# Optimization experiments

Hardware: AMD Instinct MI355X
Metric: run time of the kernel (lower is better)

The kernel has to match this reference:

```python
import jax, jax.numpy as jnp
import numpy as np

EPS = 1e-6

def setup_inputs() -> dict:
    key = jax.random.key(0)
    k1, k2 = jax.random.split(key)
    shape = (20, 1, 128, 128, 128)
    # BCE requires x strictly in (0,1); keep away from endpoints like a sigmoid output.
    x = jax.random.uniform(k1, shape, dtype=jnp.float32, minval=EPS, maxval=1.0 - EPS)
    y = jax.random.uniform(k2, shape, dtype=jnp.float32, minval=0.0, maxval=1.0)
    return {"x": x, "y": y}

def reference(x, y):
    # binary_cross_entropy (mean reduction); torch clamps log terms at -100
    log_x = jnp.clip(jnp.log(x), -100.0)
    log_1mx = jnp.clip(jnp.log1p(-x), -100.0)
    mseloss = -jnp.mean(y * log_x + (1.0 - y) * log_1mx)

    # threshold prediction at 0.5 -> {0,1}; truncate target to int (floor toward 0)
    xb = jnp.where(x > 0.5, 1, 0)              # int
    yb = y.astype(jnp.int32)                   # astype(int) truncation

    B = x.shape[0]  # loop is over range(20); batch == 20
    por_pred = jnp.mean((xb == 0).astype(jnp.float32).reshape(B, -1), axis=1)
    por_true = jnp.mean((yb == 0).astype(jnp.float32).reshape(B, -1), axis=1)
    PORE = jnp.mean((por_pred - por_true) ** 2)  # sum over 20 samples / 20

    return (PORE + mseloss, PORE)
```

## Files before the change

kernel.cpp:

```cpp
#include <hip/hip_runtime.h>

#define NBATCH 20
#define ELEMS_PER_BATCH (128 * 128 * 128)
#define BLOCKS_PER_BATCH 128
#define THREADS 256
#define V4_PER_THREAD 16
#define NPART (NBATCH * BLOCKS_PER_BATCH)

#define LN2 0.69314718055994530942
#define LOG2_CLAMP (-144.26950408889634f)

__global__ __launch_bounds__(THREADS) void partial_kernel(
    const float* __restrict__ x, const float* __restrict__ y,
    float* __restrict__ bce_part, int* __restrict__ pred_part,
    int* __restrict__ true_part) {
  const int b   = blockIdx.y;
  const int seg = blockIdx.x;
  const int tid = threadIdx.x;

  const long base4 = (long)b * (ELEMS_PER_BATCH / 4) +
                     (long)seg * (THREADS * V4_PER_THREAD);
  const float4* __restrict__ x4 = (const float4*)x;
  const float4* __restrict__ y4 = (const float4*)y;

  float bce2 = 0.0f;
  int pc = 0, tc = 0;

#pragma unroll
  for (int k = 0; k < V4_PER_THREAD; ++k) {
    const long idx = base4 + (long)k * THREADS + tid;
    const float4 xv = x4[idx];
    const float4 yv = y4[idx];

#pragma unroll
    for (int c = 0; c < 4; ++c) {
      const float xx = (c == 0) ? xv.x : (c == 1) ? xv.y : (c == 2) ? xv.z : xv.w;
      const float yy = (c == 0) ? yv.x : (c == 1) ? yv.y : (c == 2) ? yv.z : yv.w;
      const float lx = fmaxf(__builtin_amdgcn_logf(xx),        LOG2_CLAMP);
      const float l1 = fmaxf(__builtin_amdgcn_logf(1.0f - xx), LOG2_CLAMP);
      bce2 += l1 + yy * (lx - l1);
      pc += (xx <= 0.5f);
      tc += (yy < 1.0f);
    }
  }

  __shared__ float sb[THREADS];
  __shared__ int   sp[THREADS];
  __shared__ int   st[THREADS];
  sb[tid] = bce2; sp[tid] = pc; st[tid] = tc;
  __syncthreads();
#pragma unroll
  for (int s = THREADS / 2; s > 0; s >>= 1) {
    if (tid < s) {
      sb[tid] += sb[tid + s];
      sp[tid] += sp[tid + s];
      st[tid] += st[tid + s];
    }
    __syncthreads();
  }
  if (tid == 0) {
    const int o = b * BLOCKS_PER_BATCH + seg;
    bce_part[o]  = (float)(sb[0] * LN2);
    pred_part[o] = sp[0];
    true_part[o] = st[0];
  }
}

__global__ __launch_bounds__(THREADS) void final_kernel(
    const float* __restrict__ bce_part, const int* __restrict__ pred_part,
    const int* __restrict__ true_part, float* __restrict__ out) {
  const int tid = threadIdx.x;
  __shared__ double sred[THREADS];
  __shared__ float  spor[NBATCH];

  double local = 0.0;
  for (int i = tid; i < NPART; i += THREADS) local += (double)bce_part[i];
  sred[tid] = local;
  __syncthreads();
#pragma unroll
  for (int s = THREADS / 2; s > 0; s >>= 1) {
    if (tid < s) sred[tid] += sred[tid + s];
    __syncthreads();
  }

  if (tid < NBATCH) {
    int pc = 0, tc = 0;
    for (int k = 0; k < BLOCKS_PER_BATCH; ++k) {
      pc += pred_part[tid * BLOCKS_PER_BATCH + k];
      tc += true_part[tid * BLOCKS_PER_BATCH + k];
    }
    const float pp = (float)pc / (float)ELEMS_PER_BATCH;
    const float pt = (float)tc / (float)ELEMS_PER_BATCH;
    const float d = pp - pt;
    spor[tid] = d * d;
  }
  __syncthreads();

  if (tid == 0) {
    float pore_sum = 0.0f;
#pragma unroll
    for (int b = 0; b < NBATCH; ++b) pore_sum += spor[b];
    const float pore = pore_sum / (float)NBATCH;
    const double total = (double)NBATCH * (double)ELEMS_PER_BATCH;
    const float mse = (float)(-(sred[0] / total));
    out[0] = pore + mse;
    out[1] = pore;
  }
}

extern "C" void kernel_launch(void* const* d_in, const int* in_sizes, int n_in,
                              void* d_out, int out_size, void* d_ws, size_t ws_size,
                              hipStream_t stream) {
  const float* x = (const float*)d_in[0];
  const float* y = (const float*)d_in[1];
  float* out = (float*)d_out;

  float* bce_part  = (float*)d_ws;
  int*   pred_part = (int*)(bce_part + NPART);
  int*   true_part = pred_part + NPART;

  dim3 grid(BLOCKS_PER_BATCH, NBATCH);
  partial_kernel<<<grid, THREADS, 0, stream>>>(x, y, bce_part, pred_part, true_part);
  final_kernel<<<1, THREADS, 0, stream>>>(bce_part, pred_part, true_part, out);
}
```

Before: 338.4 us.

## Double-buffer register loads and halve blocks per batch

Each block now processes twice as much data (64 blocks per batch, 32 float4 per thread). The loads go through an explicit two-buffer register pipeline: the next batch of four float4 pairs is issued before the current batch is computed. The intent is to overlap memory latency with the log computation and to cut per-block reduction overhead. In exchange there are fewer blocks in flight and register pressure rises, which may reduce occupancy.

```diff
diff --git a/kernel.cpp b/kernel.cpp
--- a/kernel.cpp
+++ b/kernel.cpp
@@ -2,13 +2,44 @@
 
 #define NBATCH 20
 #define ELEMS_PER_BATCH (128 * 128 * 128)
-#define BLOCKS_PER_BATCH 128
+#define BLOCKS_PER_BATCH 64
 #define THREADS 256
-#define V4_PER_THREAD 16
+#define BAT 4
+#define NSTEP 8
 #define NPART (NBATCH * BLOCKS_PER_BATCH)
 
 #define LN2 0.69314718055994530942
 #define LOG2_CLAMP (-144.26950408889634f)
+
+__device__ __forceinline__ void load_batch(const float4* __restrict__ x4,
+                                           const float4* __restrict__ y4,
+                                           long base, int tid,
+                                           float4 (&bx)[BAT], float4 (&by)[BAT]) {
+#pragma unroll
+  for (int j = 0; j < BAT; ++j) {
+    const long idx = base + (long)j * THREADS + tid;
+    bx[j] = x4[idx];
+    by[j] = y4[idx];
+  }
+}
+
+__device__ __forceinline__ void compute_batch(const float4 (&bx)[BAT],
+                                              const float4 (&by)[BAT],
+                                              float& bce2, int& pc, int& tc) {
+#pragma unroll
+  for (int j = 0; j < BAT; ++j) {
+#pragma unroll
+    for (int c = 0; c < 4; ++c) {
+      const float xx = (c == 0) ? bx[j].x : (c == 1) ? bx[j].y : (c == 2) ? bx[j].z : bx[j].w;
+      const float yy = (c == 0) ? by[j].x : (c == 1) ? by[j].y : (c == 2) ? by[j].z : by[j].w;
+      const float lx = fmaxf(__builtin_amdgcn_logf(xx),        LOG2_CLAMP);
+      const float l1 = fmaxf(__builtin_amdgcn_logf(1.0f - xx), LOG2_CLAMP);
+      bce2 += l1 + yy * (lx - l1);
+      pc += (xx <= 0.5f);
+      tc += (yy < 1.0f);
+    }
+  }
+}
 
 __global__ __launch_bounds__(THREADS) void partial_kernel(
     const float* __restrict__ x, const float* __restrict__ y,
@@ -19,30 +50,30 @@
   const int tid = threadIdx.x;
 
   const long base4 = (long)b * (ELEMS_PER_BATCH / 4) +
-                     (long)seg * (THREADS * V4_PER_THREAD);
+                     (long)seg * (BAT * NSTEP * THREADS);
   const float4* __restrict__ x4 = (const float4*)x;
   const float4* __restrict__ y4 = (const float4*)y;
 
   float bce2 = 0.0f;
   int pc = 0, tc = 0;
 
-#pragma unroll
-  for (int k = 0; k < V4_PER_THREAD; ++k) {
-    const long idx = base4 + (long)k * THREADS + tid;
-    const float4 xv = x4[idx];
-    const float4 yv = y4[idx];
+  float4 ax[BAT], ay[BAT], bx[BAT], by[BAT];
+  load_batch(x4, y4, base4, tid, ax, ay);
 
-#pragma unroll
-    for (int c = 0; c < 4; ++c) {
-      const float xx = (c == 0) ? xv.x : (c == 1) ? xv.y : (c == 2) ? xv.z : xv.w;
-      const float yy = (c == 0) ? yv.x : (c == 1) ? yv.y : (c == 2) ? yv.z : yv.w;
-      const float lx = fmaxf(__builtin_amdgcn_logf(xx),        LOG2_CLAMP);
-      const float l1 = fmaxf(__builtin_amdgcn_logf(1.0f - xx), LOG2_CLAMP);
-      bce2 += l1 + yy * (lx - l1);
-      pc += (xx <= 0.5f);
-      tc += (yy < 1.0f);
-    }
-  }
+#define PIPE_STEP(CX, CY, NX, NY, S)                                           \
+  if ((S) + 1 < NSTEP)                                                         \
+    load_batch(x4, y4, base4 + (long)((S) + 1) * (BAT * THREADS), tid, NX, NY);\
+  compute_batch(CX, CY, bce2, pc, tc);
+
+  PIPE_STEP(ax, ay, bx, by, 0)
+  PIPE_STEP(bx, by, ax, ay, 1)
+  PIPE_STEP(ax, ay, bx, by, 2)
+  PIPE_STEP(bx, by, ax, ay, 3)
+  PIPE_STEP(ax, ay, bx, by, 4)
+  PIPE_STEP(bx, by, ax, ay, 5)
+  PIPE_STEP(ax, ay, bx, by, 6)
+  PIPE_STEP(bx, by, ax, ay, 7)
+#undef PIPE_STEP
 
   __shared__ float sb[THREADS];
   __shared__ int   sp[THREADS];
```

Result: no change. 337.4 us (-0.3%).

## Restructure partial reduction to stride across batches with software-pipelined nontemporal loads

Applied to the files above, without the earlier changes.

Each thread now handles one float4 position in every one of the 20 batches. It double-buffers the loads so the next batch's data is fetched while the current batch is computed, and the loads use nontemporal hints. Per-batch counts are packed into one int, reduced within each wavefront by shuffles, and summed through shared-memory atomics. The final kernel is reworked to sum the packed per-batch partials. This is meant to improve memory-level parallelism and cut shared-memory reduction work, at the cost of more partials and atomics and strided batch access.

```diff
diff --git a/kernel.cpp b/kernel.cpp
--- a/kernel.cpp
+++ b/kernel.cpp
@@ -2,79 +2,94 @@
 
 #define NBATCH 20
 #define ELEMS_PER_BATCH (128 * 128 * 128)
-#define BLOCKS_PER_BATCH 128
+#define BATCH_F4 (ELEMS_PER_BATCH / 4)
 #define THREADS 256
-#define V4_PER_THREAD 16
-#define NPART (NBATCH * BLOCKS_PER_BATCH)
+#define GRID_BLOCKS 2048
 
 #define LN2 0.69314718055994530942
 #define LOG2_CLAMP (-144.26950408889634f)
 
-__global__ __launch_bounds__(THREADS) void partial_kernel(
+typedef float f4 __attribute__((ext_vector_type(4)));
+
+
+__global__ __launch_bounds__(THREADS, 8) void partial_kernel(
     const float* __restrict__ x, const float* __restrict__ y,
-    float* __restrict__ bce_part, int* __restrict__ pred_part,
-    int* __restrict__ true_part) {
-  const int b   = blockIdx.y;
-  const int seg = blockIdx.x;
+    float* __restrict__ bce_part, int* __restrict__ comb_part) {
   const int tid = threadIdx.x;
+  const int gid = blockIdx.x * THREADS + tid;
 
-  const long base4 = (long)b * (ELEMS_PER_BATCH / 4) +
-                     (long)seg * (THREADS * V4_PER_THREAD);
-  const float4* __restrict__ x4 = (const float4*)x;
-  const float4* __restrict__ y4 = (const float4*)y;
+  const f4* __restrict__ x4 = (const f4*)x;
+  const f4* __restrict__ y4 = (const f4*)y;
+
+  __shared__ int sc[NBATCH];
+  if (tid < NBATCH) sc[tid] = 0;
+  __syncthreads();
 
   float bce2 = 0.0f;
-  int pc = 0, tc = 0;
 
-#pragma unroll
-  for (int k = 0; k < V4_PER_THREAD; ++k) {
-    const long idx = base4 + (long)k * THREADS + tid;
-    const float4 xv = x4[idx];
-    const float4 yv = y4[idx];
+  f4 xa, ya, xb, yb;
+  xa = __builtin_nontemporal_load(&x4[gid]);
+  ya = __builtin_nontemporal_load(&y4[gid]);
 
-#pragma unroll
-    for (int c = 0; c < 4; ++c) {
-      const float xx = (c == 0) ? xv.x : (c == 1) ? xv.y : (c == 2) ? xv.z : xv.w;
-      const float yy = (c == 0) ? yv.x : (c == 1) ? yv.y : (c == 2) ? yv.z : yv.w;
-      const float lx = fmaxf(__builtin_amdgcn_logf(xx),        LOG2_CLAMP);
-      const float l1 = fmaxf(__builtin_amdgcn_logf(1.0f - xx), LOG2_CLAMP);
-      bce2 += l1 + yy * (lx - l1);
-      pc += (xx <= 0.5f);
-      tc += (yy < 1.0f);
-    }
+#define PROCESS(XV, YV, S)                                                     \
+  {                                                                            \
+    int pc = 0, tc = 0;                                                        \
+    _Pragma("unroll")                                                          \
+    for (int c = 0; c < 4; ++c) {                                              \
+      const float xx = XV[c];                                                  \
+      const float yy = YV[c];                                                  \
+      const float lx = fmaxf(__builtin_amdgcn_logf(xx),        LOG2_CLAMP);    \
+      const float l1 = fmaxf(__builtin_amdgcn_logf(1.0f - xx), LOG2_CLAMP);    \
+      bce2 += l1 + yy * (lx - l1);                          \
+      pc += (xx <= 0.5f);                                                      \
+      tc += (yy < 1.0f);                                                       \
+    }                                                                          \
+    int packed = pc | (tc << 16); \
+    _Pragma("unroll")                                                          \
+    for (int o = 32; o > 0; o >>= 1) packed += __shfl_xor(packed, o);          \
+    if ((tid & 63) == 0) atomicAdd(&sc[S], packed);                            \
   }
 
+#define STEP(CX, CY, NX, NY, S)                                                \
+  if ((S) + 1 < NBATCH) {                                                      \
+    NX = __builtin_nontemporal_load(&x4[((S) + 1) * BATCH_F4 + gid]);          \
+    NY = __builtin_nontemporal_load(&y4[((S) + 1) * BATCH_F4 + gid]);          \
+  }                                                                            \
+  PROCESS(CX, CY, S)
+
+  STEP(xa, ya, xb, yb, 0)   STEP(xb, yb, xa, ya, 1)
+  STEP(xa, ya, xb, yb, 2)   STEP(xb, yb, xa, ya, 3)
+  STEP(xa, ya, xb, yb, 4)   STEP(xb, yb, xa, ya, 5)
+  STEP(xa, ya, xb, yb, 6)   STEP(xb, yb, xa, ya, 7)
+  STEP(xa, ya, xb, yb, 8)   STEP(xb, yb, xa, ya, 9)
+  STEP(xa, ya, xb, yb, 10)  STEP(xb, yb, xa, ya, 11)
+  STEP(xa, ya, xb, yb, 12)  STEP(xb, yb, xa, ya, 13)
+  STEP(xa, ya, xb, yb, 14)  STEP(xb, yb, xa, ya, 15)
+  STEP(xa, ya, xb, yb, 16)  STEP(xb, yb, xa, ya, 17)
+  STEP(xa, ya, xb, yb, 18)  STEP(xb, yb, xa, ya, 19)
+#undef STEP
+#undef PROCESS
+
   __shared__ float sb[THREADS];
-  __shared__ int   sp[THREADS];
-  __shared__ int   st[THREADS];
-  sb[tid] = bce2; sp[tid] = pc; st[tid] = tc;
+  sb[tid] = bce2;
   __syncthreads();
 #pragma unroll
   for (int s = THREADS / 2; s > 0; s >>= 1) {
-    if (tid < s) {
-      sb[tid] += sb[tid + s];
-      sp[tid] += sp[tid + s];
-      st[tid] += st[tid + s];
-    }
+    if (tid < s) sb[tid] += sb[tid + s];
     __syncthreads();
   }
-  if (tid == 0) {
-    const int o = b * BLOCKS_PER_BATCH + seg;
-    bce_part[o]  = (float)(sb[0] * LN2);
-    pred_part[o] = sp[0];
-    true_part[o] = st[0];
-  }
+  if (tid == 0) bce_part[blockIdx.x] = sb[0] * (float)LN2;
+  if (tid < NBATCH) comb_part[tid * GRID_BLOCKS + blockIdx.x] = sc[tid];
 }
 
 __global__ __launch_bounds__(THREADS) void final_kernel(
-    const float* __restrict__ bce_part, const int* __restrict__ pred_part,
-    const int* __restrict__ true_part, float* __restrict__ out) {
+    const float* __restrict__ bce_part, const int* __restrict__ comb_part,
+    float* __restrict__ out) {
   const int tid = threadIdx.x;
+
   __shared__ double sred[THREADS];
-  __shared__ float  spor[NBATCH];
-
   double local = 0.0;
-  for (int i = tid; i < NPART; i += THREADS) local += (double)bce_part[i];
+  for (int i = tid; i < GRID_BLOCKS; i += THREADS) local += (double)bce_part[i];
   sred[tid] = local;
   __syncthreads();
 #pragma unroll
@@ -83,14 +98,30 @@
     __syncthreads();
   }
 
+  __shared__ int pcb[NBATCH], tcb[NBATCH];
+  if (tid < NBATCH) { pcb[tid] = 0; tcb[tid] = 0; }
+  __syncthreads();
+  for (int s = 0; s < NBATCH; ++s) {
+    int pl = 0, tl = 0;
+    for (int i = tid; i < GRID_BLOCKS; i += THREADS) {
+      const int c = comb_part[s * GRID_BLOCKS + i];
+      pl += c & 0xFFFF;
+      tl += (c >> 16) & 0xFFFF;
+    }
+    long long packed = (long long)pl | ((long long)tl << 32);
+#pragma unroll
+    for (int o = 32; o > 0; o >>= 1) packed += __shfl_xor(packed, o);
+    if ((tid & 63) == 0) {
+      atomicAdd(&pcb[s], (int)(packed & 0xFFFFFFFFll));
+      atomicAdd(&tcb[s], (int)(packed >> 32));
+    }
+  }
+  __syncthreads();
+
+  __shared__ float spor[NBATCH];
   if (tid < NBATCH) {
-    int pc = 0, tc = 0;
-    for (int k = 0; k < BLOCKS_PER_BATCH; ++k) {
-      pc += pred_part[tid * BLOCKS_PER_BATCH + k];
-      tc += true_part[tid * BLOCKS_PER_BATCH + k];
-    }
-    const float pp = (float)pc / (float)ELEMS_PER_BATCH;
-    const float pt = (float)tc / (float)ELEMS_PER_BATCH;
+    const float pp = (float)pcb[tid] / (float)ELEMS_PER_BATCH;
+    const float pt = (float)tcb[tid] / (float)ELEMS_PER_BATCH;
     const float d = pp - pt;
     spor[tid] = d * d;
   }
@@ -116,10 +147,8 @@
   float* out = (float*)d_out;
 
   float* bce_part  = (float*)d_ws;
-  int*   pred_part = (int*)(bce_part + NPART);
-  int*   true_part = pred_part + NPART;
+  int*   comb_part = (int*)(bce_part + GRID_BLOCKS);
 
-  dim3 grid(BLOCKS_PER_BATCH, NBATCH);
-  partial_kernel<<<grid, THREADS, 0, stream>>>(x, y, bce_part, pred_part, true_part);
-  final_kernel<<<1, THREADS, 0, stream>>>(bce_part, pred_part, true_part, out);
+  partial_kernel<<<GRID_BLOCKS, THREADS, 0, stream>>>(x, y, bce_part, comb_part);
+  final_kernel<<<1, THREADS, 0, stream>>>(bce_part, comb_part, out);
 }
```

New measurement: 435.1 us. 28.6% more time.

## Double-buffer global-to-LDS async loads and use wave-shuffle block reduction

Applied to the files above, without the earlier changes.

Each block now covers twice the data (64 blocks per batch) and streams x and y through a double-buffered LDS tile using global_load_lds direct-to-LDS copies, with explicit vmcnt waits so the loads of tile t+2 overlap the compute on tile t. The shared-memory tree reduction is replaced by wave-level shuffles followed by a four-entry cross-wave combine that reuses the tile buffers. The aim is to keep more memory traffic in flight and cut the cost of the reduction. The risks are fewer blocks in the grid, more LDS per block lowering occupancy, and the extra LDS round-trip. Correctness also depends on the hand-written waitcnt counts being right.

```diff
diff --git a/kernel.cpp b/kernel.cpp
--- a/kernel.cpp
+++ b/kernel.cpp
@@ -2,13 +2,22 @@
 
 #define NBATCH 20
 #define ELEMS_PER_BATCH (128 * 128 * 128)
-#define BLOCKS_PER_BATCH 128
+#define BLOCKS_PER_BATCH 64
 #define THREADS 256
-#define V4_PER_THREAD 16
+#define TILE_F4 512
+#define NTILE 16
 #define NPART (NBATCH * BLOCKS_PER_BATCH)
 
 #define LN2 0.69314718055994530942
 #define LOG2_CLAMP (-144.26950408889634f)
+
+typedef float f4 __attribute__((ext_vector_type(4)));
+typedef const __attribute__((address_space(1))) unsigned int gu32;
+typedef __attribute__((address_space(3)))       unsigned int lu32;
+
+__device__ __forceinline__ void stage16(const f4* g, f4* l) {
+  __builtin_amdgcn_global_load_lds((gu32*)g, (lu32*)l, 16, 0, 2);
+}
 
 __global__ __launch_bounds__(THREADS) void partial_kernel(
     const float* __restrict__ x, const float* __restrict__ y,
@@ -19,50 +28,91 @@
   const int tid = threadIdx.x;
 
   const long base4 = (long)b * (ELEMS_PER_BATCH / 4) +
-                     (long)seg * (THREADS * V4_PER_THREAD);
-  const float4* __restrict__ x4 = (const float4*)x;
-  const float4* __restrict__ y4 = (const float4*)y;
+                     (long)seg * (NTILE * TILE_F4);
+  const f4* __restrict__ x4 = (const f4*)x;
+  const f4* __restrict__ y4 = (const f4*)y;
+
+  __shared__ f4 lx[2][TILE_F4];
+  __shared__ f4 ly[2][TILE_F4];
 
   float bce2 = 0.0f;
   int pc = 0, tc = 0;
 
-#pragma unroll
-  for (int k = 0; k < V4_PER_THREAD; ++k) {
-    const long idx = base4 + (long)k * THREADS + tid;
-    const float4 xv = x4[idx];
-    const float4 yv = y4[idx];
-
-#pragma unroll
-    for (int c = 0; c < 4; ++c) {
-      const float xx = (c == 0) ? xv.x : (c == 1) ? xv.y : (c == 2) ? xv.z : xv.w;
-      const float yy = (c == 0) ? yv.x : (c == 1) ? yv.y : (c == 2) ? yv.z : yv.w;
-      const float lx = fmaxf(__builtin_amdgcn_logf(xx),        LOG2_CLAMP);
-      const float l1 = fmaxf(__builtin_amdgcn_logf(1.0f - xx), LOG2_CLAMP);
-      bce2 += l1 + yy * (lx - l1);
-      pc += (xx <= 0.5f);
-      tc += (yy < 1.0f);
-    }
+#define STAGE(T, B)                                                            \
+  {                                                                            \
+    const long tb = base4 + (long)(T) * TILE_F4;                               \
+    stage16(&x4[tb + tid],       &lx[B][tid]);                                 \
+    stage16(&x4[tb + 256 + tid], &lx[B][256 + tid]);                           \
+    stage16(&y4[tb + tid],       &ly[B][tid]);                                 \
+    stage16(&y4[tb + 256 + tid], &ly[B][256 + tid]);                           \
   }
 
-  __shared__ float sb[THREADS];
-  __shared__ int   sp[THREADS];
-  __shared__ int   st[THREADS];
-  sb[tid] = bce2; sp[tid] = pc; st[tid] = tc;
+#define PH(T, B, VM)                                                           \
+  asm volatile("s_waitcnt vmcnt(" #VM ")" ::: "memory");                       \
+  __builtin_amdgcn_sched_barrier(0);                                           \
+  {                                                                            \
+    _Pragma("unroll")                                                          \
+    for (int j = 0; j < 2; ++j) {                                              \
+      const f4 xv = lx[B][j * 256 + tid];                                      \
+      const f4 yv = ly[B][j * 256 + tid];                                      \
+      _Pragma("unroll")                                                        \
+      for (int c = 0; c < 4; ++c) {                                            \
+        const float xx = xv[c];                                                \
+        const float yy = yv[c];                                                \
+        const float lg = fmaxf(__builtin_amdgcn_logf(xx),        LOG2_CLAMP);  \
+        const float l1 = fmaxf(__builtin_amdgcn_logf(1.0f - xx), LOG2_CLAMP);  \
+        bce2 += l1 + yy * (lg - l1);                      \
+        pc += (xx <= 0.5f);                                                    \
+        tc += (yy < 1.0f);                                                     \
+      }                                                                        \
+    }                                                                          \
+  }
+
+  STAGE(0, 0)
+  STAGE(1, 1)
+  PH(0, 0, 4)  STAGE(2, 0)
+  PH(1, 1, 4)  STAGE(3, 1)
+  PH(2, 0, 4)  STAGE(4, 0)
+  PH(3, 1, 4)  STAGE(5, 1)
+  PH(4, 0, 4)  STAGE(6, 0)
+  PH(5, 1, 4)  STAGE(7, 1)
+  PH(6, 0, 4)  STAGE(8, 0)
+  PH(7, 1, 4)  STAGE(9, 1)
+  PH(8, 0, 4)  STAGE(10, 0)
+  PH(9, 1, 4)  STAGE(11, 1)
+  PH(10, 0, 4) STAGE(12, 0)
+  PH(11, 1, 4) STAGE(13, 1)
+  PH(12, 0, 4) STAGE(14, 0)
+  PH(13, 1, 4) STAGE(15, 1)
+  PH(14, 0, 4)
+  PH(15, 1, 0)
+#undef STAGE
+#undef PH
+
+  float wb = bce2;
+  int   wp = pc, wt = tc;
+#pragma unroll
+  for (int o = 32; o > 0; o >>= 1) {
+    wb += __shfl_down(wb, o);
+    wp += __shfl_down(wp, o);
+    wt += __shfl_down(wt, o);
+  }
   __syncthreads();
-#pragma unroll
-  for (int s = THREADS / 2; s > 0; s >>= 1) {
-    if (tid < s) {
-      sb[tid] += sb[tid + s];
-      sp[tid] += sp[tid + s];
-      st[tid] += st[tid + s];
-    }
-    __syncthreads();
+  float* sb = (float*)&lx[0][0];
+  int*   sp = (int*)&lx[1][0];
+  int*   st = (int*)&ly[0][0];
+  if ((tid & 63) == 0) {
+    sb[tid >> 6] = wb;
+    sp[tid >> 6] = wp;
+    st[tid >> 6] = wt;
   }
+  __syncthreads();
   if (tid == 0) {
+    const float bsum = (sb[0] + sb[1]) + (sb[2] + sb[3]);
     const int o = b * BLOCKS_PER_BATCH + seg;
-    bce_part[o]  = (float)(sb[0] * LN2);
-    pred_part[o] = sp[0];
-    true_part[o] = st[0];
+    bce_part[o]  = bsum * (float)LN2;
+    pred_part[o] = sp[0] + sp[1] + sp[2] + sp[3];
+    true_part[o] = st[0] + st[1] + st[2] + st[3];
   }
 }
 
```

Result: faster. 307.9 us (-9.0%).
